# Performance work log

Measured on AMD Instinct MI355X. Metric: run time of the kernel, lower is better.

The kernel has to match this reference:

```python
import jax, jax.numpy as jnp
import numpy as np

B, A, V, D = 16, 1024, 512, 512
TEMPERATURE = 1.0
NEG = jnp.float32(-1e30)  # stand-in for -inf (avoids inf-inf NaNs in grads)
EPS = 1e-12               # F.normalize eps


def setup_inputs() -> dict:
    key = jax.random.key(0)
    k1, k2, k3 = jax.random.split(key, 3)
    audio_features = jax.random.normal(k1, (B, A, D), jnp.float32)
    video_features = jax.random.normal(k2, (B, V, D), jnp.float32)
    W = jax.random.normal(k3, (D, D), jnp.float32) / np.sqrt(D)  # nn.Linear weight [out,in]
    b = jnp.zeros((D,), jnp.float32)
    return {"audio_features": audio_features, "video_features": video_features, "W": W, "b": b}


def _normalize(x):
    n = jnp.linalg.norm(x, axis=-1, keepdims=True)
    return x / jnp.maximum(n, EPS)


def _dtw_score(sim):
    # sim: [B, A, V]. dp[i,j] = sim[i-1,j-1] + max(dp[i-1,j], dp[i,j-1], dp[i-1,j-1]).
    Bn, An, Vn = sim.shape
    init_row = jnp.full((Bn, Vn + 1), NEG).at[:, 0].set(0.0)  # dp row 0

    def row_step(prev_row, cost_row):
        # prev_row: [B, V+1], cost_row: [B, V]
        def col_step(left, xs):
            c, up, diag = xs  # each [B]
            val = c + jnp.maximum(jnp.maximum(up, left), diag)
            return val, val

        xs = (cost_row.T, prev_row[:, 1:].T, prev_row[:, :-1].T)  # [V, B] each
        _, vals = jax.lax.scan(col_step, jnp.full((Bn,), NEG), xs)  # vals: [V, B]
        new_row = jnp.concatenate([jnp.full((Bn, 1), NEG), vals.T], axis=1)
        return new_row, None

    final_row, _ = jax.lax.scan(row_step, init_row, jnp.swapaxes(sim, 0, 1))
    return final_row[:, -1]  # dp[:, A, V]


def reference(audio_features, video_features, W, b):
    audio_proj = jnp.einsum('bad,ed->bae', audio_features, W) + b
    video_proj = jnp.einsum('bvd,ed->bve', video_features, W) + b
    a_n = _normalize(audio_proj)
    v_n = _normalize(video_proj)
    similarity = jnp.einsum('bad,bvd->bav', a_n, v_n) / TEMPERATURE  # [B, A, V]
    alignment_score = _dtw_score(similarity)                          # [B]
    path_prob = jax.nn.softmax(similarity, axis=-1)
    aligned_video = jnp.einsum('bav,bvd->bad', path_prob, video_features)  # [B, A, D]
    return aligned_video, alignment_score
```

## Files before the change

kernel.cpp:

```cpp
#include <hip/hip_runtime.h>
#include <math.h>

#define B_DIM 16
#define A_DIM 1024
#define V_DIM 512
#define D_DIM 512
#define NEGV  (-1e30f)
#define SKT_W 768

typedef short bf16x8 __attribute__((ext_vector_type(8)));
typedef float floatx4 __attribute__((ext_vector_type(4)));

__device__ __forceinline__ short bf16_rne(float f) {
    unsigned u = __float_as_uint(f);
    return (short)((u + 0x7fffu + ((u >> 16) & 1u)) >> 16);
}

__device__ __forceinline__ float max3f(float a, float b, float c) {
    float d;
    asm("v_max3_f32 %0, %1, %2, %3" : "=v"(d) : "v"(a), "v"(b), "v"(c));
    return d;
}

__global__ __launch_bounds__(256) void cvt3_bf16_kernel(
    const float* __restrict__ in0, unsigned short* __restrict__ out0, int nb0,
    const float* __restrict__ in1, unsigned short* __restrict__ out1, int nb1,
    const float* __restrict__ in2, unsigned short* __restrict__ out2)
{
    int blk = blockIdx.x;
    const float* in; unsigned short* out;
    if (blk < nb0)              { in = in0; out = out0; }
    else if (blk < nb0 + nb1)   { in = in1; out = out1; blk -= nb0; }
    else                        { in = in2; out = out2; blk -= nb0 + nb1; }
    const int i = blk * 256 + threadIdx.x;
    float4 u = ((const float4*)in)[2*i];
    float4 v = ((const float4*)in)[2*i + 1];
    bf16x8 h;
    h[0]=bf16_rne(u.x); h[1]=bf16_rne(u.y); h[2]=bf16_rne(u.z); h[3]=bf16_rne(u.w);
    h[4]=bf16_rne(v.x); h[5]=bf16_rne(v.y); h[6]=bf16_rne(v.z); h[7]=bf16_rne(v.w);
    *(bf16x8*)(out + (size_t)i * 8) = h;
}

__device__ __forceinline__ void gemm_tile_body(
    const unsigned short* __restrict__ Ab, const unsigned short* __restrict__ Bb,
    const float* __restrict__ bias, float* __restrict__ Cb,
    int m0, int n0, int K, int N,
    unsigned short* lA, unsigned short* lB)
{
    const int tid = threadIdx.x, lane = tid & 63;
    const int w = tid >> 6, wy = w >> 1, wx = w & 1;

    const int u0 = tid, u1 = tid + 256;
    const int r_u0 = ((u0 >> 6) << 4) + (u0 & 15), k_u0 = ((u0 >> 4) & 3) * 8;
    const int r_u1 = ((u1 >> 6) << 4) + (u1 & 15), k_u1 = ((u1 >> 4) & 3) * 8;

    const unsigned short* gA0 = Ab + (size_t)(m0 + r_u0) * K + k_u0;
    const unsigned short* gA1 = Ab + (size_t)(m0 + r_u1) * K + k_u1;
    const unsigned short* gB0 = Bb + (size_t)(n0 + r_u0) * K + k_u0;
    const unsigned short* gB1 = Bb + (size_t)(n0 + r_u1) * K + k_u1;

    floatx4 acc[4][4];
    #pragma unroll
    for (int i = 0; i < 4; ++i)
        #pragma unroll
        for (int j = 0; j < 4; ++j) acc[i][j] = (floatx4){0.f, 0.f, 0.f, 0.f};

    bf16x8 a0 = *(const bf16x8*)(gA0);
    bf16x8 a1 = *(const bf16x8*)(gA1);
    bf16x8 b0 = *(const bf16x8*)(gB0);
    bf16x8 b1 = *(const bf16x8*)(gB1);

    for (int k0 = 0; k0 < K; k0 += 32) {
        __syncthreads();
        *(bf16x8*)&lA[(size_t)u0 * 8] = a0;
        *(bf16x8*)&lA[(size_t)u1 * 8] = a1;
        *(bf16x8*)&lB[(size_t)u0 * 8] = b0;
        *(bf16x8*)&lB[(size_t)u1 * 8] = b1;
        __syncthreads();

        if (k0 + 32 < K) {
            a0 = *(const bf16x8*)(gA0 + k0 + 32);
            a1 = *(const bf16x8*)(gA1 + k0 + 32);
            b0 = *(const bf16x8*)(gB0 + k0 + 32);
            b1 = *(const bf16x8*)(gB1 + k0 + 32);
        }

        bf16x8 fa[4], fb[4];
        #pragma unroll
        for (int t = 0; t < 4; ++t) {
            fa[t] = *(const bf16x8*)&lA[(((wy*4 + t)*64) + lane) * 8];
            fb[t] = *(const bf16x8*)&lB[(((wx*4 + t)*64) + lane) * 8];
        }
        #pragma unroll
        for (int i = 0; i < 4; ++i)
            #pragma unroll
            for (int j = 0; j < 4; ++j)
                acc[i][j] = __builtin_amdgcn_mfma_f32_16x16x32_bf16(fa[i], fb[j], acc[i][j], 0, 0, 0);
    }

    const int q = lane >> 4, c = lane & 15;
    #pragma unroll
    for (int i = 0; i < 4; ++i)
        #pragma unroll
        for (int j = 0; j < 4; ++j) {
            const int n = n0 + (wx*4 + j)*16 + c;
            const float bv = bias ? bias[n] : 0.f;
            #pragma unroll
            for (int r = 0; r < 4; ++r) {
                const int m = m0 + (wy*4 + i)*16 + q*4 + r;
                Cb[(size_t)m * N + n] = acc[i][j][r] + bv;
            }
        }
}

__global__ __launch_bounds__(256) void gemm_bf16_nt(
    const unsigned short* __restrict__ Ag, const unsigned short* __restrict__ Bg,
    const float* __restrict__ bias, float* __restrict__ Cg,
    int M, int N, int K, size_t strA, size_t strB, size_t strC)
{
    __shared__ __align__(16) unsigned short lA[8*64*8];
    __shared__ __align__(16) unsigned short lB[8*64*8];
    const unsigned short* Ab = Ag + (size_t)blockIdx.z * strA;
    const unsigned short* Bb = Bg + (size_t)blockIdx.z * strB;
    float*                Cb = Cg + (size_t)blockIdx.z * strC;
    gemm_tile_body(Ab, Bb, bias, Cb, blockIdx.y * 128, blockIdx.x * 128, K, N, lA, lB);
}

__global__ __launch_bounds__(256) void gemm_proj2(
    const unsigned short* __restrict__ abf, const unsigned short* __restrict__ vbf,
    const unsigned short* __restrict__ Wbf, const float* __restrict__ bias,
    float* __restrict__ a_p, float* __restrict__ v_p)
{
    __shared__ __align__(16) unsigned short lA[8*64*8];
    __shared__ __align__(16) unsigned short lB[8*64*8];
    const int by = blockIdx.y;
    const unsigned short* Ab; float* Cb; int m0;
    if (by < 128) { Ab = abf; Cb = a_p; m0 = by * 128; }
    else          { Ab = vbf; Cb = v_p; m0 = (by - 128) * 128; }
    gemm_tile_body(Ab, Wbf, bias, Cb, m0, blockIdx.x * 128, D_DIM, D_DIM, lA, lB);
}

__global__ __launch_bounds__(256) void norm2_transpose_kernel(
    const float* __restrict__ a_p, unsigned short* __restrict__ a_nb,
    const float* __restrict__ v_p, unsigned short* __restrict__ v_nb,
    const float* __restrict__ video, unsigned short* __restrict__ vTb)
{
    __shared__ float t[32][33];
    const int bx = blockIdx.x;
    if (bx < 6144) {
        const float* in; unsigned short* out; int rb;
        if (bx < 4096) { in = a_p; out = a_nb; rb = bx; }
        else           { in = v_p; out = v_nb; rb = bx - 4096; }
        const int wave = threadIdx.x >> 6;
        const int lane = threadIdx.x & 63;
        const size_t r = (size_t)rb * 4 + wave;
        const float* p = in + r * D_DIM + lane * 8;
        float4 u = *(const float4*)p;
        float4 w = *(const float4*)(p + 4);
        float ss = u.x*u.x + u.y*u.y + u.z*u.z + u.w*u.w
                 + w.x*w.x + w.y*w.y + w.z*w.z + w.w*w.w;
        #pragma unroll
        for (int m = 1; m < 64; m <<= 1) ss += __shfl_xor(ss, m, 64);
        const float inv = 1.0f / fmaxf(sqrtf(ss), 1e-12f);
        bf16x8 h;
        h[0]=bf16_rne(u.x*inv); h[1]=bf16_rne(u.y*inv); h[2]=bf16_rne(u.z*inv); h[3]=bf16_rne(u.w*inv);
        h[4]=bf16_rne(w.x*inv); h[5]=bf16_rne(w.y*inv); h[6]=bf16_rne(w.z*inv); h[7]=bf16_rne(w.w*inv);
        *(bf16x8*)(out + r * D_DIM + lane * 8) = h;
    } else {
        const int tt = bx - 6144;
        const int d0 = (tt & 15) * 32;
        const int v0 = ((tt >> 4) & 15) * 32;
        const int b  = tt >> 8;
        const int x = threadIdx.x & 31, y0 = (threadIdx.x >> 5) * 4;
        const float* I = video + ((size_t)b * V_DIM + v0) * D_DIM + d0;
        #pragma unroll
        for (int r = 0; r < 4; ++r) t[y0 + r][x] = I[(size_t)(y0 + r) * D_DIM + x];
        __syncthreads();
        unsigned short* O = vTb + ((size_t)b * D_DIM + d0) * V_DIM + v0;
        #pragma unroll
        for (int r = 0; r < 4; ++r) O[(size_t)(y0 + r) * V_DIM + x] = (unsigned short)bf16_rne(t[x][y0 + r]);
    }
}

template <int CTRL, int RMASK>
__device__ __forceinline__ float fdpp(float oldv, float src) {
    int r = __builtin_amdgcn_update_dpp(
        __float_as_int(oldv), __float_as_int(src), CTRL, RMASK, 0xF, false);
    return __int_as_float(r);
}

__global__ __launch_bounds__(256) void softmax_skewT_kernel(
    const float* __restrict__ sim, unsigned short* __restrict__ Pbf,
    float* __restrict__ skewT)
{
    __shared__ float tl[4][520];
    const int wave = threadIdx.x >> 6;
    const int lane = threadIdx.x & 63;
    const size_t r = (size_t)blockIdx.x * 4 + wave;
    const float* p = sim + r * V_DIM + lane * 8;
    float4 u = *(const float4*)p;
    float4 w = *(const float4*)(p + 4);
    float s[8] = {u.x,u.y,u.z,u.w,w.x,w.y,w.z,w.w};

    float m = s[0];
    #pragma unroll
    for (int k = 1; k < 8; ++k) m = fmaxf(m, s[k]);
    #pragma unroll
    for (int t = 1; t < 64; t <<= 1) m = fmaxf(m, __shfl_xor(m, t, 64));

    const float L2E = 1.44269504f;
    float ex[8];
    float e = 0.f;
    #pragma unroll
    for (int k = 0; k < 8; ++k) { ex[k] = exp2f((s[k] - m) * L2E); e += ex[k]; }
    #pragma unroll
    for (int t = 1; t < 64; t <<= 1) e += __shfl_xor(e, t, 64);
    const float ri = 1.0f / e;

    bf16x8 h;
    #pragma unroll
    for (int k = 0; k < 8; ++k) h[k] = bf16_rne(ex[k] * ri);
    *(bf16x8*)(Pbf + r * V_DIM + lane * 8) = h;

    #pragma unroll
    for (int k = 0; k < 8; ++k) tl[wave][lane * 8 + k] = s[k];
    __syncthreads();

    const int r0 = blockIdx.x * 4;
    const int b  = r0 >> 10;
    const int i0 = r0 & 1023;
    const int g  = i0 >> 2;
    const int off = (g & 63) + 72 * (g >> 6);
    float* sbase = skewT + (size_t)b * SKT_W * 1024 + i0;
    #pragma unroll
    for (int cc = 0; cc < 2; ++cc) {
        const int c = threadIdx.x + cc * 256;
        int pc = c + off; if (pc >= SKT_W) pc -= SKT_W;
        float4 v = make_float4(tl[0][c], tl[1][c], tl[2][c], tl[3][c]);
        *(float4*)(sbase + (size_t)pc * 1024) = v;
    }
}

__global__ __launch_bounds__(256) void pv_dtw_kernel(
    const unsigned short* __restrict__ Pbf, const unsigned short* __restrict__ vTb,
    const float* __restrict__ skewT, float* __restrict__ out_aligned,
    float* __restrict__ out_score)
{
    __shared__ __align__(16) unsigned short lA[8*64*8];
    __shared__ __align__(16) unsigned short lB[8*64*8];

    if (blockIdx.x < 16) {
        const int b    = blockIdx.x;
        const int tid  = threadIdx.x;
        const int lane = tid & 63;
        const int wv   = tid >> 6;
        const int off  = lane + 72 * wv;

        float* bndAll = (float*)lA;
        float* bndP = bndAll + wv * 520;
        const float* bndC = bndAll + (wv > 0 ? wv - 1 : 0) * 520;
        for (int i = tid; i < 3 * 520; i += 256) bndAll[i] = NEGV;
        __syncthreads();

        const float* Sb = skewT + (size_t)b * SKT_W * 1024 + 4 * tid;

        float dp[4] = {NEGV, NEGV, NEGV, NEGV};
        float st[8];
        float upC = NEGV;
        float upL = (tid == 0) ? 0.0f : NEGV;

        float4 CA[8], CB[8];
        #pragma unroll
        for (int k = 0; k < 8; ++k) CA[k] = *(const float4*)(Sb + (size_t)k * 1024);
        #pragma unroll
        for (int k = 0; k < 8; ++k) CB[k] = *(const float4*)(Sb + (size_t)(k + 8) * 1024);

#define DTW_STEP(K, CK, FK)                                                   \
        {                                                                     \
            const unsigned jj = (unsigned)(sb + (K) - off);                   \
            if (jj < 512u) {                                                  \
                float u = upC, g = upL, old, nd;                              \
                old = dp[0]; nd = (CK).x + max3f(u, dp[0], g); dp[0] = nd; g = old; u = nd; \
                old = dp[1]; nd = (CK).y + max3f(u, dp[1], g); dp[1] = nd; g = old; u = nd; \
                old = dp[2]; nd = (CK).z + max3f(u, dp[2], g); dp[2] = nd; g = old; u = nd; \
                old = dp[3]; nd = (CK).w + max3f(u, dp[3], g); dp[3] = nd;                  \
            }                                                                 \
            st[K] = dp[3];                                                    \
            upL = upC;                                                        \
            upC = fdpp<0x138, 0xF>((FK), dp[3]);                              \
        }

#define DTW_BATCH(CC)                                                         \
        {                                                                     \
            float4 f0, f1;                                                    \
            const int ps = sb + 8 - 72 * wv;                                  \
            if (wv > 0 && ps >= 0 && ps <= 512) {                             \
                f0 = *(const float4*)&bndC[ps];                               \
                f1 = *(const float4*)&bndC[ps + 4];                           \
            } else {                                                          \
                f0 = make_float4(NEGV, NEGV, NEGV, NEGV); f1 = f0;            \
            }                                                                 \
            DTW_STEP(0, CC[0], f0.x) DTW_STEP(1, CC[1], f0.y)                 \
            DTW_STEP(2, CC[2], f0.z) DTW_STEP(3, CC[3], f0.w)                 \
            DTW_STEP(4, CC[4], f1.x) DTW_STEP(5, CC[5], f1.y)                 \
            DTW_STEP(6, CC[6], f1.z) DTW_STEP(7, CC[7], f1.w)                 \
            {                                                                 \
                _Pragma("unroll")                                             \
                for (int k = 0; k < 8; ++k) {                                 \
                    int cc_ = sb + 16 + k; if (cc_ >= SKT_W) cc_ -= SKT_W;    \
                    CC[k] = *(const float4*)(Sb + (size_t)cc_ * 1024);        \
                }                                                             \
            }                                                                 \
            if (wv < 3 && lane == 63) {                                       \
                _Pragma("unroll")                                             \
                for (int k = 0; k < 8; ++k) {                                 \
                    const int jp = sb + k - 63 - 72 * wv;                     \
                    const int adr = ((unsigned)jp < 512u) ? (jp + 7) : 519;   \
                    bndP[adr] = st[k];                                        \
                }                                                             \
            }                                                                 \
            asm volatile("s_waitcnt lgkmcnt(0)" ::: "memory");                \
            __builtin_amdgcn_s_barrier();                                     \
            asm volatile("" ::: "memory");                                    \
        }

        #pragma unroll 1
        for (int bt = 0; bt < 100; bt += 2) {
            int sb = bt * 8;
            DTW_BATCH(CA)
            sb += 8;
            DTW_BATCH(CB)
        }
#undef DTW_BATCH
#undef DTW_STEP
        if (tid == 255) out_score[b] = dp[3];
        return;
    }

    const int bid = blockIdx.x - 16;
    const int n0 = (bid & 3) * 128;
    const int m0 = ((bid >> 2) & 7) * 128;
    const int bz = bid >> 5;

    const unsigned short* Ab = Pbf + (size_t)bz * A_DIM * V_DIM;
    const unsigned short* Bb = vTb + (size_t)bz * V_DIM * D_DIM;
    float*                Cb = out_aligned + (size_t)bz * A_DIM * D_DIM;

    gemm_tile_body(Ab, Bb, nullptr, Cb, m0, n0, V_DIM, D_DIM, lA, lB);
}

extern "C" void kernel_launch(void* const* d_in, const int* in_sizes, int n_in,
                              void* d_out, int out_size, void* d_ws, size_t ws_size,
                              hipStream_t stream)
{
    const float* audio = (const float*)d_in[0];
    const float* video = (const float*)d_in[1];
    const float* W     = (const float*)d_in[2];
    const float* bias  = (const float*)d_in[3];

    float* out_aligned = (float*)d_out;
    float* out_score   = (float*)d_out + (size_t)B_DIM * A_DIM * D_DIM;

    const size_t NA = (size_t)B_DIM * A_DIM * D_DIM;
    const size_t NV = (size_t)B_DIM * V_DIM * D_DIM;
    const size_t NS = (size_t)B_DIM * A_DIM * V_DIM;

    float* ws = (float*)d_ws;
    float*          a_p  = ws;
    float*          v_p  = a_p + NA;
    float*          sim  = v_p + NV;
    unsigned short* abf  = (unsigned short*)(sim + NS);
    unsigned short* vbf  = (unsigned short*)(sim + NS) + NA;
    unsigned short* v_nb = vbf + NV;
    unsigned short* Wbf  = v_nb + NV;
    unsigned short* a_nb = abf;
    unsigned short* Pbf  = abf;
    unsigned short* vTb  = vbf;
    float*          skewT = a_p;

    {
        const int nb_a = (int)(NA / 8 / 256);
        const int nb_v = (int)(NV / 8 / 256);
        const int nb_w = D_DIM * D_DIM / 8 / 256;
        cvt3_bf16_kernel<<<dim3(nb_a + nb_v + nb_w), dim3(256), 0, stream>>>(
            audio, abf, nb_a, video, vbf, nb_v, W, Wbf);
    }

    gemm_proj2<<<dim3(D_DIM/128, 192), dim3(256), 0, stream>>>(
        abf, vbf, Wbf, bias, a_p, v_p);

    norm2_transpose_kernel<<<dim3(4096 + 2048 + 4096), dim3(256), 0, stream>>>(
        a_p, a_nb, v_p, v_nb, video, vTb);

    gemm_bf16_nt<<<dim3(V_DIM/128, A_DIM/128, B_DIM), dim3(256), 0, stream>>>(
        a_nb, v_nb, nullptr, sim, A_DIM, V_DIM, D_DIM,
        (size_t)A_DIM*D_DIM, (size_t)V_DIM*D_DIM, (size_t)A_DIM*V_DIM);

    softmax_skewT_kernel<<<dim3((B_DIM*A_DIM)/4), dim3(256), 0, stream>>>(sim, Pbf, skewT);

    pv_dtw_kernel<<<dim3(16 + (D_DIM/128)*(A_DIM/128)*B_DIM), dim3(256), 0, stream>>>(
        Pbf, vTb, skewT, out_aligned, out_score);
}
```

Before: 284.5 us.

## Double DTW batch depth and pack two batches or GEMM tiles per block

The DTW wavefront now processes 16 anti-diagonal columns between block barriers instead of 8, so there are half as many barrier and LDS-boundary exchanges on the serial critical path. The skew stride between waves grows from 72 to 80, and the prefetch buffers double to four float4[8] sets. Blocks become 512 threads: each block runs either two batches' DTW or two PV GEMM tiles, with shared memory split between the halves. The cost is much higher register pressure under a 512-thread launch bound, which risks spills, plus longer per-wave lag from the wider skew.

```diff
diff --git a/kernel.cpp b/kernel.cpp
--- a/kernel.cpp
+++ b/kernel.cpp
@@ -44,10 +44,10 @@
 __device__ __forceinline__ void gemm_tile_body(
     const unsigned short* __restrict__ Ab, const unsigned short* __restrict__ Bb,
     const float* __restrict__ bias, float* __restrict__ Cb,
-    int m0, int n0, int K, int N,
+    int m0, int n0, int K, int N, int tid,
     unsigned short* lA, unsigned short* lB)
 {
-    const int tid = threadIdx.x, lane = tid & 63;
+    const int lane = tid & 63;
     const int w = tid >> 6, wy = w >> 1, wx = w & 1;
 
     const int u0 = tid, u1 = tid + 256;
@@ -123,7 +123,8 @@
     const unsigned short* Ab = Ag + (size_t)blockIdx.z * strA;
     const unsigned short* Bb = Bg + (size_t)blockIdx.z * strB;
     float*                Cb = Cg + (size_t)blockIdx.z * strC;
-    gemm_tile_body(Ab, Bb, bias, Cb, blockIdx.y * 128, blockIdx.x * 128, K, N, lA, lB);
+    gemm_tile_body(Ab, Bb, bias, Cb, blockIdx.y * 128, blockIdx.x * 128, K, N,
+                   threadIdx.x, lA, lB);
 }
 
 __global__ __launch_bounds__(256) void gemm_proj2(
@@ -137,7 +138,8 @@
     const unsigned short* Ab; float* Cb; int m0;
     if (by < 128) { Ab = abf; Cb = a_p; m0 = by * 128; }
     else          { Ab = vbf; Cb = v_p; m0 = (by - 128) * 128; }
-    gemm_tile_body(Ab, Wbf, bias, Cb, m0, blockIdx.x * 128, D_DIM, D_DIM, lA, lB);
+    gemm_tile_body(Ab, Wbf, bias, Cb, m0, blockIdx.x * 128, D_DIM, D_DIM,
+                   threadIdx.x, lA, lB);
 }
 
 __global__ __launch_bounds__(256) void norm2_transpose_kernel(
@@ -230,7 +232,7 @@
     const int b  = r0 >> 10;
     const int i0 = r0 & 1023;
     const int g  = i0 >> 2;
-    const int off = (g & 63) + 72 * (g >> 6);
+    const int off = (g & 63) + 80 * (g >> 6);
     float* sbase = skewT + (size_t)b * SKT_W * 1024 + i0;
     #pragma unroll
     for (int cc = 0; cc < 2; ++cc) {
@@ -241,39 +243,43 @@
     }
 }
 
-__global__ __launch_bounds__(256) void pv_dtw_kernel(
+__global__ __launch_bounds__(512) void pv_dtw_kernel(
     const unsigned short* __restrict__ Pbf, const unsigned short* __restrict__ vTb,
     const float* __restrict__ skewT, float* __restrict__ out_aligned,
     float* __restrict__ out_score)
 {
-    __shared__ __align__(16) unsigned short lA[8*64*8];
-    __shared__ __align__(16) unsigned short lB[8*64*8];
-
-    if (blockIdx.x < 16) {
-        const int b    = blockIdx.x;
-        const int tid  = threadIdx.x;
+    __shared__ __align__(16) unsigned short shmem_u16[16384];
+
+    const int half = threadIdx.x >> 8;
+    const int tid  = threadIdx.x & 255;
+
+    if (blockIdx.x < 8) {
+        const int b    = blockIdx.x * 2 + half;
         const int lane = tid & 63;
         const int wv   = tid >> 6;
-        const int off  = lane + 72 * wv;
-
-        float* bndAll = (float*)lA;
-        float* bndP = bndAll + wv * 520;
-        const float* bndC = bndAll + (wv > 0 ? wv - 1 : 0) * 520;
-        for (int i = tid; i < 3 * 520; i += 256) bndAll[i] = NEGV;
+        const int off  = lane + 80 * wv;
+
+        float* bndAll = (float*)shmem_u16 + half * (3 * 528);
+        float* bndP = bndAll + wv * 528;
+        const float* bndC = bndAll + (wv > 0 ? wv - 1 : 0) * 528;
+        for (int i = tid; i < 3 * 528; i += 256) bndAll[i] = NEGV;
         __syncthreads();
 
         const float* Sb = skewT + (size_t)b * SKT_W * 1024 + 4 * tid;
 
         float dp[4] = {NEGV, NEGV, NEGV, NEGV};
-        float st[8];
+        float st[16];
         float upC = NEGV;
         float upL = (tid == 0) ? 0.0f : NEGV;
 
-        float4 CA[8], CB[8];
-        #pragma unroll
-        for (int k = 0; k < 8; ++k) CA[k] = *(const float4*)(Sb + (size_t)k * 1024);
-        #pragma unroll
-        for (int k = 0; k < 8; ++k) CB[k] = *(const float4*)(Sb + (size_t)(k + 8) * 1024);
+        float4 CA[8], CB[8], CC[8], CD[8];
+        #pragma unroll
+        for (int k = 0; k < 8; ++k) {
+            CA[k] = *(const float4*)(Sb + (size_t)k * 1024);
+            CB[k] = *(const float4*)(Sb + (size_t)(k + 8) * 1024);
+            CC[k] = *(const float4*)(Sb + (size_t)(k + 16) * 1024);
+            CD[k] = *(const float4*)(Sb + (size_t)(k + 24) * 1024);
+        }
 
 #define DTW_STEP(K, CK, FK)                                                   \
         {                                                                     \
@@ -290,32 +296,38 @@
             upC = fdpp<0x138, 0xF>((FK), dp[3]);                              \
         }
 
-#define DTW_BATCH(CC)                                                         \
+#define DTW_BATCH16(P, Q)                                                     \
         {                                                                     \
-            float4 f0, f1;                                                    \
-            const int ps = sb + 8 - 72 * wv;                                  \
-            if (wv > 0 && ps >= 0 && ps <= 512) {                             \
-                f0 = *(const float4*)&bndC[ps];                               \
-                f1 = *(const float4*)&bndC[ps + 4];                           \
-            } else {                                                          \
-                f0 = make_float4(NEGV, NEGV, NEGV, NEGV); f1 = f0;            \
+            const int ps = sb + 8 - 80 * wv;                                  \
+            float f[16];                                                      \
+            _Pragma("unroll")                                                 \
+            for (int k = 0; k < 16; ++k) {                                    \
+                int idx = ps + k;                                             \
+                idx = idx < 0 ? 0 : (idx > 527 ? 527 : idx);                  \
+                f[k] = (wv > 0) ? bndC[idx] : NEGV;                           \
             }                                                                 \
-            DTW_STEP(0, CC[0], f0.x) DTW_STEP(1, CC[1], f0.y)                 \
-            DTW_STEP(2, CC[2], f0.z) DTW_STEP(3, CC[3], f0.w)                 \
-            DTW_STEP(4, CC[4], f1.x) DTW_STEP(5, CC[5], f1.y)                 \
-            DTW_STEP(6, CC[6], f1.z) DTW_STEP(7, CC[7], f1.w)                 \
+            DTW_STEP(0,  P[0], f[0])  DTW_STEP(1,  P[1], f[1])                \
+            DTW_STEP(2,  P[2], f[2])  DTW_STEP(3,  P[3], f[3])                \
+            DTW_STEP(4,  P[4], f[4])  DTW_STEP(5,  P[5], f[5])                \
+            DTW_STEP(6,  P[6], f[6])  DTW_STEP(7,  P[7], f[7])                \
+            DTW_STEP(8,  Q[0], f[8])  DTW_STEP(9,  Q[1], f[9])                \
+            DTW_STEP(10, Q[2], f[10]) DTW_STEP(11, Q[3], f[11])               \
+            DTW_STEP(12, Q[4], f[12]) DTW_STEP(13, Q[5], f[13])               \
+            DTW_STEP(14, Q[6], f[14]) DTW_STEP(15, Q[7], f[15])               \
             {                                                                 \
                 _Pragma("unroll")                                             \
                 for (int k = 0; k < 8; ++k) {                                 \
-                    int cc_ = sb + 16 + k; if (cc_ >= SKT_W) cc_ -= SKT_W;    \
-                    CC[k] = *(const float4*)(Sb + (size_t)cc_ * 1024);        \
+                    int c1 = sb + 32 + k; if (c1 >= SKT_W) c1 -= SKT_W;       \
+                    P[k] = *(const float4*)(Sb + (size_t)c1 * 1024);          \
+                    int c2 = sb + 40 + k; if (c2 >= SKT_W) c2 -= SKT_W;       \
+                    Q[k] = *(const float4*)(Sb + (size_t)c2 * 1024);          \
                 }                                                             \
             }                                                                 \
             if (wv < 3 && lane == 63) {                                       \
                 _Pragma("unroll")                                             \
-                for (int k = 0; k < 8; ++k) {                                 \
-                    const int jp = sb + k - 63 - 72 * wv;                     \
-                    const int adr = ((unsigned)jp < 512u) ? (jp + 7) : 519;   \
+                for (int k = 0; k < 16; ++k) {                                \
+                    const int jp = sb + k - 63 - 80 * wv;                     \
+                    const int adr = ((unsigned)jp < 512u) ? (jp + 7) : 527;   \
                     bndP[adr] = st[k];                                        \
                 }                                                             \
             }                                                                 \
@@ -325,28 +337,30 @@
         }
 
         #pragma unroll 1
-        for (int bt = 0; bt < 100; bt += 2) {
-            int sb = bt * 8;
-            DTW_BATCH(CA)
-            sb += 8;
-            DTW_BATCH(CB)
-        }
-#undef DTW_BATCH
+        for (int bt = 0; bt < 52; bt += 2) {
+            int sb = bt * 16;
+            DTW_BATCH16(CA, CB)
+            sb += 16;
+            DTW_BATCH16(CC, CD)
+        }
+#undef DTW_BATCH16
 #undef DTW_STEP
         if (tid == 255) out_score[b] = dp[3];
         return;
     }
 
-    const int bid = blockIdx.x - 16;
-    const int n0 = (bid & 3) * 128;
-    const int m0 = ((bid >> 2) & 7) * 128;
-    const int bz = bid >> 5;
+    const int tile = (blockIdx.x - 8) * 2 + half;
+    const int n0 = (tile & 3) * 128;
+    const int m0 = ((tile >> 2) & 7) * 128;
+    const int bz = tile >> 5;
 
     const unsigned short* Ab = Pbf + (size_t)bz * A_DIM * V_DIM;
     const unsigned short* Bb = vTb + (size_t)bz * V_DIM * D_DIM;
     float*                Cb = out_aligned + (size_t)bz * A_DIM * D_DIM;
 
-    gemm_tile_body(Ab, Bb, nullptr, Cb, m0, n0, V_DIM, D_DIM, lA, lB);
+    unsigned short* lA = shmem_u16 + half * 8192;
+    unsigned short* lB = lA + 4096;
+    gemm_tile_body(Ab, Bb, nullptr, Cb, m0, n0, V_DIM, D_DIM, tid, lA, lB);
 }
 
 extern "C" void kernel_launch(void* const* d_in, const int* in_sizes, int n_in,
@@ -398,6 +412,6 @@
 
     softmax_skewT_kernel<<<dim3((B_DIM*A_DIM)/4), dim3(256), 0, stream>>>(sim, Pbf, skewT);
 
-    pv_dtw_kernel<<<dim3(16 + (D_DIM/128)*(A_DIM/128)*B_DIM), dim3(256), 0, stream>>>(
+    pv_dtw_kernel<<<dim3(8 + 256), dim3(512), 0, stream>>>(
         Pbf, vTb, skewT, out_aligned, out_score);
 }
```

New measurement: 329.0 us. 15.7% more time.
